# Performance work log

Hardware: AMD Instinct MI355X
Metric: run time of the kernel (lower is better)

Reference implementation:

```python
import jax, jax.numpy as jnp
import numpy as np
from jax import lax

IMG_SIZE = 640
STRIDES = (8, 16, 32)
NA = 3          # anchors per level
NC = 80         # classes
CONF_THRESH = 0.001
NMS_THRESH = 0.6
ANCHORS = np.array([[10,13],[16,30],[33,23],[30,61],[62,45],[59,119],[116,90],[156,198],[373,326]], np.float32).reshape(3, 3, 2)

def _make_grids():
    gs, st, aw = [], [], []
    for i, s in enumerate(STRIDES):
        hs = ws = IMG_SIZE // s
        gy, gx = np.meshgrid(np.arange(hs), np.arange(ws), indexing='ij')
        gxy = np.stack([gx, gy], -1).astype(np.float32).reshape(1, hs*ws, 1, 2)
        gs.append(gxy)
        st.append(np.full((1, hs*ws, NA, 2), s, np.float32))
        aw.append(np.tile(ANCHORS[i][None], (hs*ws, 1, 1)))
    return (np.concatenate(gs, 1), np.concatenate(st, 1), np.concatenate(aw, 0)[None])

GRID_CELL, STRIDE_T, ANCH_WH = _make_grids()  # [1,HW,1,2], [1,HW,3,2], [1,HW,3,2]

def _nms_classaware(boxes, score, valid):
    # Greedy NMS, class-aware via coordinate offset already applied to boxes.
    # Faithful to the numpy baseline: w,h = max(1e-28, .), areas without +1.
    x1, y1, x2, y2 = boxes[:, 0], boxes[:, 1], boxes[:, 2], boxes[:, 3]
    areas = (x2 - x1) * (y2 - y1)
    order = jnp.argsort(-score)
    N = boxes.shape[0]
    def body(i, state):
        supp, keep = state
        idx = order[i]
        active = jnp.logical_and(jnp.logical_not(supp[idx]), valid[idx])
        keep = keep.at[idx].set(active)
        xx1 = jnp.maximum(x1[idx], x1)
        yy1 = jnp.maximum(y1[idx], y1)
        xx2 = jnp.minimum(x2[idx], x2)
        yy2 = jnp.minimum(y2[idx], y2)
        w = jnp.maximum(1e-28, xx2 - xx1)
        h = jnp.maximum(1e-28, yy2 - yy1)
        inter = w * h
        iou = inter / (areas[idx] + areas - inter)
        newsupp = jnp.logical_and(iou > NMS_THRESH, active)
        newsupp = newsupp.at[idx].set(False)
        return jnp.logical_or(supp, newsupp), keep
    supp0 = jnp.zeros((N,), bool)
    keep0 = jnp.zeros((N,), bool)
    _, keep = lax.fori_loop(0, N, body, (supp0, keep0))
    return keep

def _decode_and_nms(pred_s, pred_m, pred_l):
    objs, clss, regs = [], [], []
    for pred in (pred_s, pred_m, pred_l):
        B, C, H, W = pred.shape
        p = pred.transpose(0, 2, 3, 1).reshape(B, H*W, C)
        objs.append(p[..., :NA].reshape(B, H*W*NA, 1))
        clss.append(p[..., NA:NA*(1+NC)].reshape(B, H*W*NA, NC))
        regs.append(p[..., NA*(1+NC):].reshape(B, H*W, NA, 4))
    obj_pred = jnp.concatenate(objs, axis=1)   # [B, N, 1]
    cls_pred = jnp.concatenate(clss, axis=1)   # [B, N, NC]
    reg_pred = jnp.concatenate(regs, axis=1)   # [B, HW, 3, 4]
    grid = jnp.asarray(GRID_CELL)
    stride = jnp.asarray(STRIDE_T)
    anch = jnp.asarray(ANCH_WH)
    B = reg_pred.shape[0]
    c_xy = (jax.nn.sigmoid(reg_pred[..., :2]) + grid) * stride
    b_wh = jnp.exp(reg_pred[..., 2:]) * anch
    xywh = jnp.concatenate([c_xy, b_wh], -1).reshape(B, -1, 4)
    x1y1 = xywh[..., :2] - xywh[..., 2:] / 2
    x2y2 = xywh[..., :2] + xywh[..., 2:] / 2
    boxes = jnp.clip(jnp.concatenate([x1y1, x2y2], -1) / IMG_SIZE, 0.0, 1.0)[0]  # [N,4]
    obj_s = jax.nn.sigmoid(obj_pred)[0]                     # [N,1]
    scores_all = jax.nn.softmax(cls_pred[0], axis=1) * obj_s  # [N,NC]
    cls_ind = jnp.argmax(scores_all, axis=1)                # [N]
    score = jnp.max(scores_all, axis=1)                     # [N]
    valid = score >= CONF_THRESH
    # class-aware NMS: offset normalized boxes by 2*class so classes never overlap
    boxes_off = boxes + cls_ind[:, None].astype(boxes.dtype) * 2.0
    keep = _nms_classaware(lax.stop_gradient(boxes_off), lax.stop_gradient(score), valid)
    out = jnp.concatenate([
        boxes,                                    # 4 cols
        score[:, None],                           # 1 col
        cls_ind[:, None].astype(boxes.dtype),     # 1 col (non-diff)
        keep[:, None].astype(boxes.dtype),        # 1 col (non-diff)
    ], axis=1)                                    # [N, 7]
    return out

def setup_inputs() -> dict:
    key = jax.random.key(0)
    k1, k2, k3 = jax.random.split(key, 3)
    return {
        'pred_s': jax.random.normal(k1, (1, 255, 80, 80), jnp.float32),
        'pred_m': jax.random.normal(k2, (1, 255, 40, 40), jnp.float32),
        'pred_l': jax.random.normal(k3, (1, 255, 20, 20), jnp.float32),
    }

def reference(pred_s, pred_m, pred_l):
    return _decode_and_nms(pred_s, pred_m, pred_l)
```

## Files before the change

kernel.cpp:

```cpp
#include <hip/hip_runtime.h>
#include <cstdint>

#define NPRED 25200
#define NPOS  8400
#define NCLS  80
#define CAP   512
#define MW    8
#define NCHUNK 132

__device__ __forceinline__ float sigmoidf_(float x) { return 1.0f / (1.0f + expf(-x)); }

__global__ __launch_bounds__(64) void decode_kernel(
    const float* __restrict__ ps, const float* __restrict__ pm, const float* __restrict__ pl,
    float* __restrict__ out,
    float4* __restrict__ g_boxin, uint64_t* __restrict__ g_key)
{
    int chunk = blockIdx.x;
    int a     = blockIdx.y;
    int t     = threadIdx.x;

    const float* p; int HW, W, base, si; float stride; int w0;
    if (chunk < 100)      { p = ps; HW = 6400; W = 80; stride = 8.f;  base = 0;    si = 0; w0 = chunk * 64; }
    else if (chunk < 125) { p = pm; HW = 1600; W = 40; stride = 16.f; base = 6400; si = 1; w0 = (chunk - 100) * 64; }
    else                  { p = pl; HW = 400;  W = 20; stride = 32.f; base = 8000; si = 2; w0 = (chunk - 125) * 64; }

    int local = w0 + t;
    bool valid = local < HW;
    int lclamp = valid ? local : (HW - 1);

    __shared__ float lds[NCLS * 64];

    const float* cbase = p + (size_t)(3 + a * NCLS) * HW;
    int lane_c = t >> 4;
    int j      = (t & 15) << 2;
    int off    = w0 + j; if (off > HW - 4) off = HW - 4;

    float4 vreg[20];
#pragma unroll
    for (int r0 = 0; r0 < 20; r0++)
        vreg[r0] = *(const float4*)(cbase + (size_t)(r0 * 4 + lane_c) * HW + off);
    float objl = p[(size_t)a * HW + lclamp];
    const float* rb = p + (size_t)(3 + 3 * NCLS + a * 4) * HW + lclamp;
    float tx = rb[0], ty = rb[(size_t)HW], tw = rb[(size_t)2 * HW], th = rb[(size_t)3 * HW];
#pragma unroll
    for (int r0 = 0; r0 < 20; r0++)
        *(float4*)&lds[(r0 * 4 + lane_c) * 64 + j] = vreg[r0];
    __syncthreads();

    float m = -INFINITY;
#pragma unroll 16
    for (int c = 0; c < NCLS; c++) m = fmaxf(m, lds[c * 64 + t]);
    float s = 0.f; float beste = -1.f; int bi = 0;
#pragma unroll 16
    for (int c = 0; c < NCLS; c++) {
        float e = expf(lds[c * 64 + t] - m);
        s += e;
        if (e > beste) { beste = e; bi = c; }
    }
    float obj = sigmoidf_(objl);
    float best = beste / s * obj;

    if (!valid) return;

    const float AW[9] = {10.f,16.f,33.f, 30.f,62.f,59.f, 116.f,156.f,373.f};
    const float AH[9] = {13.f,30.f,23.f, 61.f,45.f,119.f, 90.f,198.f,326.f};
    float aw = AW[si*3 + a], ah = AH[si*3 + a];

    int y = local / W;
    int x = local - y * W;
    float cx = (sigmoidf_(tx) + (float)x) * stride;
    float cy = (sigmoidf_(ty) + (float)y) * stride;
    float bw = expf(tw) * aw;
    float bh = expf(th) * ah;
    float x1 = fminf(fmaxf((cx - bw / 2.f) / 640.f, 0.f), 1.f);
    float y1 = fminf(fmaxf((cy - bh / 2.f) / 640.f, 0.f), 1.f);
    float x2 = fminf(fmaxf((cx + bw / 2.f) / 640.f, 0.f), 1.f);
    float y2 = fminf(fmaxf((cy + bh / 2.f) / 640.f, 0.f), 1.f);

    int g = (base + local) * 3 + a;
    float clsf = (float)bi;
    float* o = out + (size_t)g * 7;
    o[0] = x1; o[1] = y1; o[2] = x2; o[3] = y2;
    o[4] = best; o[5] = clsf; o[6] = 0.f;

    if (best >= 0.001f) {
        float off2 = clsf * 2.0f;
        g_boxin[g] = make_float4(x1 + off2, y1 + off2, x2 + off2, y2 + off2);
        unsigned u = __float_as_uint(best);
        u = (u & 0x80000000u) ? ~u : (u | 0x80000000u);
        g_key[g] = ((uint64_t)bi << 47) | ((uint64_t)(~u) << 15) | (uint64_t)g;
    } else {
        g_key[g] = (uint64_t)127 << 47;
    }
}

__global__ __launch_bounds__(1024, 4) void nms_fused_kernel(
    const uint64_t* __restrict__ g_key, const float4* __restrict__ g_boxin,
    float* __restrict__ out)
{
    int c = blockIdx.x;
    int tid = threadIdx.x;

    __shared__ uint64_t key_s[CAP];
    __shared__ float4   boxu_s[CAP];
    __shared__ float4   sbox_s[CAP + 64];
    __shared__ int      sg_s[CAP];
    __shared__ uint64_t mask_s[MW * CAP];
    __shared__ int      ln_s;

    if (tid == 0) ln_s = 0;
    __syncthreads();

    {
        int lane = tid & 63;
        const ulonglong2* kp = (const ulonglong2*)g_key;
        for (int idx = tid; idx < NPRED / 2; idx += 1024) {
            ulonglong2 kv = kp[idx];
            bool m0 = (int)(kv.x >> 47) == c;
            bool m1 = (int)(kv.y >> 47) == c;
            unsigned long long b0 = __ballot(m0);
            unsigned long long b1 = __ballot(m1);
            int total = __popcll(b0) + __popcll(b1);
            int base = 0;
            if (lane == 0 && total) base = atomicAdd(&ln_s, total);
            base = __shfl(base, 0);
            unsigned long long lower = ((unsigned long long)1 << lane) - 1;
            int off0 = base + __popcll(b0 & lower);
            int off1 = base + __popcll(b0) + __popcll(b1 & lower);
            if (m0 && off0 < CAP) key_s[off0] = kv.x;
            if (m1 && off1 < CAP) key_s[off1] = kv.y;
        }
    }
    __syncthreads();
    int n = ln_s; if (n > CAP) n = CAP;
    if (n == 0) return;
    int nw = (n + 63) >> 6;

    for (int i = tid; i < n; i += 1024)
        boxu_s[i] = g_boxin[key_s[i] & 0x7FFF];
    for (int i = n + tid; i < n + 64; i += 1024)
        sbox_s[i] = make_float4(3e30f, 3e30f, 3e30f, 3e30f);
    __syncthreads();

    for (int i0 = 0; i0 < n; i0 += 256) {
        int item = i0 + (tid >> 2);
        int sub  = tid & 3;
        bool act = item < n;
        int r = 0;
        uint64_t k = 0;
        if (act) {
            k = key_s[item];
            int nq = (n + 3) >> 2;
            int lo = sub * nq; if (lo > n) lo = n;
            int hi = lo + nq;  if (hi > n) hi = n;
            int jj = lo;
            for (; jj + 8 <= hi; jj += 8) {
                int t0 = key_s[jj]   < k, t1 = key_s[jj+1] < k;
                int t2 = key_s[jj+2] < k, t3 = key_s[jj+3] < k;
                int t4 = key_s[jj+4] < k, t5 = key_s[jj+5] < k;
                int t6 = key_s[jj+6] < k, t7 = key_s[jj+7] < k;
                r += t0 + t1 + t2 + t3 + t4 + t5 + t6 + t7;
            }
            for (; jj < hi; jj++) r += (key_s[jj] < k);
        }
        r += __shfl_xor(r, 1);
        r += __shfl_xor(r, 2);
        if (act && sub == 0) {
            sbox_s[r] = boxu_s[item];
            sg_s[r]   = (int)(k & 0x7FFF);
        }
    }
    __syncthreads();

    {
        int wid   = tid >> 6;
        int lane2 = tid & 63;
        int T = nw * (nw + 1) / 2;
        for (int t = wid; t < T; t += 16) {
            int w = 0, acc = 0;
            while (t >= acc + w + 1) { acc += w + 1; w++; }
            int ib = t - acc;
            int i  = (ib << 6) + lane2;
            float4 b4 = sbox_s[i];
            float Ai = (b4.z - b4.x) * (b4.w - b4.y);
            int j0 = w << 6;
            uint64_t bits = 0;
#pragma unroll 8
            for (int jq = 0; jq < 64; jq++) {
                float4 bj = sbox_s[j0 + jq];
                float xx1 = fmaxf(b4.x, bj.x);
                float yy1 = fmaxf(b4.y, bj.y);
                float xx2 = fminf(b4.z, bj.z);
                float yy2 = fminf(b4.w, bj.w);
                float ww = fmaxf(1e-28f, xx2 - xx1);
                float hh = fmaxf(1e-28f, yy2 - yy1);
                float inter = ww * hh;
                float Aj = (bj.z - bj.x) * (bj.w - bj.y);
                float iou = inter / ((Ai + Aj) - inter);
                if ((j0 + jq) > i && iou > 0.6f) bits |= 1ull << jq;
            }
            if (i < n) mask_s[w * CAP + i] = bits;
        }
    }
    __syncthreads();

    if (tid >= 64) return;
    int lane = tid;
    uint64_t removed = 0;
    for (int w = 0; w < nw; w++) {
        uint64_t rw = __shfl(removed, w);
        int row = (w << 6) + lane;
        uint64_t diag = (row < n) ? mask_s[w * CAP + row] : 0ull;
        int rem = n - (w << 6);
        uint64_t valid = (rem >= 64) ? ~0ull : ((1ull << rem) - 1ull);
        uint64_t nulls = __ballot(diag == 0ull);
        uint64_t cand = ~rw & valid;
        uint64_t kw = 0;
        uint64_t it = cand & ~nulls;
        while (it) {
            int b = __ffsll((unsigned long long)it) - 1;
            kw |= 1ull << b;
            uint64_t db = __shfl(diag, b);
            it &= ~db; cand &= ~db;
            it &= ~(1ull << b);
        }
        kw |= cand & nulls;

        int g  = lane >> 3;
        int wp = lane & 7;
        uint64_t acc = 0;
        if (wp >= w && wp < nw) {
            uint64_t mybits = kw & (0xFFull << (g * 8));
            while (mybits) {
                int b = __ffsll((unsigned long long)mybits) - 1;
                mybits &= mybits - 1;
                acc |= mask_s[wp * CAP + ((w << 6) + b)];
            }
        }
        acc |= __shfl_xor(acc, 8);
        acc |= __shfl_xor(acc, 16);
        acc |= __shfl_xor(acc, 32);
        if (lane < MW) removed |= acc;

        if (row < n && ((kw >> lane) & 1))
            out[(size_t)sg_s[row] * 7 + 6] = 1.0f;
    }
}

extern "C" void kernel_launch(void* const* d_in, const int* in_sizes, int n_in,
                              void* d_out, int out_size, void* d_ws, size_t ws_size,
                              hipStream_t stream) {
    const float* ps = (const float*)d_in[0];
    const float* pm = (const float*)d_in[1];
    const float* pl = (const float*)d_in[2];
    float* out = (float*)d_out;

    char* ws = (char*)d_ws;
    float4*   g_boxin = (float4*)ws;
    uint64_t* g_key   = (uint64_t*)(ws + 409600);

    decode_kernel<<<dim3(NCHUNK, 3), 64, 0, stream>>>(ps, pm, pl, out, g_boxin, g_key);
    nms_fused_kernel<<<NCLS, 1024, 0, stream>>>(g_key, g_boxin, out);
}
```

Measured before the change: 108.3 us.

## Load class logits directly to registers and micro-optimize NMS bucketing, ranking, masks

```diff
diff --git a/kernel.cpp b/kernel.cpp
--- a/kernel.cpp
+++ b/kernel.cpp
@@ -10,7 +10,7 @@
 
 __device__ __forceinline__ float sigmoidf_(float x) { return 1.0f / (1.0f + expf(-x)); }
 
-__global__ __launch_bounds__(64) void decode_kernel(
+__global__ __launch_bounds__(64, 2) void decode_kernel(
     const float* __restrict__ ps, const float* __restrict__ pm, const float* __restrict__ pl,
     float* __restrict__ out,
     float4* __restrict__ g_boxin, uint64_t* __restrict__ g_key)
@@ -28,32 +28,22 @@
     bool valid = local < HW;
     int lclamp = valid ? local : (HW - 1);
 
-    __shared__ float lds[NCLS * 64];
-
-    const float* cbase = p + (size_t)(3 + a * NCLS) * HW;
-    int lane_c = t >> 4;
-    int j      = (t & 15) << 2;
-    int off    = w0 + j; if (off > HW - 4) off = HW - 4;
-
-    float4 vreg[20];
-#pragma unroll
-    for (int r0 = 0; r0 < 20; r0++)
-        vreg[r0] = *(const float4*)(cbase + (size_t)(r0 * 4 + lane_c) * HW + off);
+    const float* cbase = p + (size_t)(3 + a * NCLS) * HW + lclamp;
+    float v[NCLS];
+#pragma unroll
+    for (int c = 0; c < NCLS; c++) v[c] = cbase[(size_t)c * HW];
+
     float objl = p[(size_t)a * HW + lclamp];
     const float* rb = p + (size_t)(3 + 3 * NCLS + a * 4) * HW + lclamp;
     float tx = rb[0], ty = rb[(size_t)HW], tw = rb[(size_t)2 * HW], th = rb[(size_t)3 * HW];
-#pragma unroll
-    for (int r0 = 0; r0 < 20; r0++)
-        *(float4*)&lds[(r0 * 4 + lane_c) * 64 + j] = vreg[r0];
-    __syncthreads();
 
     float m = -INFINITY;
-#pragma unroll 16
-    for (int c = 0; c < NCLS; c++) m = fmaxf(m, lds[c * 64 + t]);
+#pragma unroll
+    for (int c = 0; c < NCLS; c++) m = fmaxf(m, v[c]);
     float s = 0.f; float beste = -1.f; int bi = 0;
-#pragma unroll 16
+#pragma unroll
     for (int c = 0; c < NCLS; c++) {
-        float e = expf(lds[c * 64 + t] - m);
+        float e = expf(v[c] - m);
         s += e;
         if (e > beste) { beste = e; bi = c; }
     }
@@ -94,6 +84,23 @@
     }
 }
 
+#define BUCKET2(kv)                                                       \
+    {                                                                     \
+        bool m0 = (int)((kv).x >> 47) == c;                               \
+        bool m1 = (int)((kv).y >> 47) == c;                               \
+        unsigned long long b0 = __ballot(m0);                             \
+        unsigned long long b1 = __ballot(m1);                             \
+        int total = __popcll(b0) + __popcll(b1);                          \
+        int bs = 0;                                                       \
+        if (lane == 0 && total) bs = atomicAdd(&ln_s, total);             \
+        bs = __shfl(bs, 0);                                               \
+        unsigned long long lower = ((unsigned long long)1 << lane) - 1;   \
+        int off0 = bs + __popcll(b0 & lower);                             \
+        int off1 = bs + __popcll(b0) + __popcll(b1 & lower);              \
+        if (m0 && off0 < CAP) key_s[off0] = (kv).x;                       \
+        if (m1 && off1 < CAP) key_s[off1] = (kv).y;                       \
+    }
+
 __global__ __launch_bounds__(1024, 4) void nms_fused_kernel(
     const uint64_t* __restrict__ g_key, const float4* __restrict__ g_boxin,
     float* __restrict__ out)
@@ -101,7 +108,7 @@
     int c = blockIdx.x;
     int tid = threadIdx.x;
 
-    __shared__ uint64_t key_s[CAP];
+    __shared__ alignas(16) uint64_t key_s[CAP];
     __shared__ float4   boxu_s[CAP];
     __shared__ float4   sbox_s[CAP + 64];
     __shared__ int      sg_s[CAP];
@@ -114,21 +121,19 @@
     {
         int lane = tid & 63;
         const ulonglong2* kp = (const ulonglong2*)g_key;
-        for (int idx = tid; idx < NPRED / 2; idx += 1024) {
-            ulonglong2 kv = kp[idx];
-            bool m0 = (int)(kv.x >> 47) == c;
-            bool m1 = (int)(kv.y >> 47) == c;
-            unsigned long long b0 = __ballot(m0);
-            unsigned long long b1 = __ballot(m1);
-            int total = __popcll(b0) + __popcll(b1);
-            int base = 0;
-            if (lane == 0 && total) base = atomicAdd(&ln_s, total);
-            base = __shfl(base, 0);
-            unsigned long long lower = ((unsigned long long)1 << lane) - 1;
-            int off0 = base + __popcll(b0 & lower);
-            int off1 = base + __popcll(b0) + __popcll(b1 & lower);
-            if (m0 && off0 < CAP) key_s[off0] = kv.x;
-            if (m1 && off1 < CAP) key_s[off1] = kv.y;
+        const int HALF = NPRED / 2;
+        const int R2 = HALF >> 11;
+        for (int r = 0; r < R2; r++) {
+            int i0 = (r << 11) + tid;
+            ulonglong2 ka = kp[i0];
+            ulonglong2 kb = kp[i0 + 1024];
+            BUCKET2(ka);
+            BUCKET2(kb);
+        }
+        int ti = (R2 << 11) + tid;
+        if (ti < HALF) {
+            ulonglong2 ka = kp[ti];
+            BUCKET2(ka);
         }
     }
     __syncthreads();
@@ -150,18 +155,23 @@
         uint64_t k = 0;
         if (act) {
             k = key_s[item];
-            int nq = (n + 3) >> 2;
+            int nq = (((n + 3) >> 2) + 1) & ~1;
             int lo = sub * nq; if (lo > n) lo = n;
             int hi = lo + nq;  if (hi > n) hi = n;
             int jj = lo;
             for (; jj + 8 <= hi; jj += 8) {
-                int t0 = key_s[jj]   < k, t1 = key_s[jj+1] < k;
-                int t2 = key_s[jj+2] < k, t3 = key_s[jj+3] < k;
-                int t4 = key_s[jj+4] < k, t5 = key_s[jj+5] < k;
-                int t6 = key_s[jj+6] < k, t7 = key_s[jj+7] < k;
-                r += t0 + t1 + t2 + t3 + t4 + t5 + t6 + t7;
-            }
-            for (; jj < hi; jj++) r += (key_s[jj] < k);
+                ulonglong2 p0 = *(const ulonglong2*)&key_s[jj];
+                ulonglong2 p1 = *(const ulonglong2*)&key_s[jj + 2];
+                ulonglong2 p2 = *(const ulonglong2*)&key_s[jj + 4];
+                ulonglong2 p3 = *(const ulonglong2*)&key_s[jj + 6];
+                r += (p0.x < k) + (p0.y < k) + (p1.x < k) + (p1.y < k)
+                   + (p2.x < k) + (p2.y < k) + (p3.x < k) + (p3.y < k);
+            }
+            for (; jj + 2 <= hi; jj += 2) {
+                ulonglong2 p0 = *(const ulonglong2*)&key_s[jj];
+                r += (p0.x < k) + (p0.y < k);
+            }
+            if (jj < hi) r += (key_s[jj] < k);
         }
         r += __shfl_xor(r, 1);
         r += __shfl_xor(r, 2);
@@ -184,20 +194,22 @@
             float4 b4 = sbox_s[i];
             float Ai = (b4.z - b4.x) * (b4.w - b4.y);
             int j0 = w << 6;
+            float4 bjc = sbox_s[j0];
             uint64_t bits = 0;
 #pragma unroll 8
             for (int jq = 0; jq < 64; jq++) {
-                float4 bj = sbox_s[j0 + jq];
-                float xx1 = fmaxf(b4.x, bj.x);
-                float yy1 = fmaxf(b4.y, bj.y);
-                float xx2 = fminf(b4.z, bj.z);
-                float yy2 = fminf(b4.w, bj.w);
+                float4 bjn = sbox_s[j0 + ((jq + 1) & 63)];
+                float xx1 = fmaxf(b4.x, bjc.x);
+                float yy1 = fmaxf(b4.y, bjc.y);
+                float xx2 = fminf(b4.z, bjc.z);
+                float yy2 = fminf(b4.w, bjc.w);
                 float ww = fmaxf(1e-28f, xx2 - xx1);
                 float hh = fmaxf(1e-28f, yy2 - yy1);
                 float inter = ww * hh;
-                float Aj = (bj.z - bj.x) * (bj.w - bj.y);
+                float Aj = (bjc.z - bjc.x) * (bjc.w - bjc.y);
                 float iou = inter / ((Ai + Aj) - inter);
                 if ((j0 + jq) > i && iou > 0.6f) bits |= 1ull << jq;
+                bjc = bjn;
             }
             if (i < n) mask_s[w * CAP + i] = bits;
         }
@@ -230,11 +242,11 @@
         int wp = lane & 7;
         uint64_t acc = 0;
         if (wp >= w && wp < nw) {
-            uint64_t mybits = kw & (0xFFull << (g * 8));
-            while (mybits) {
-                int b = __ffsll((unsigned long long)mybits) - 1;
-                mybits &= mybits - 1;
-                acc |= mask_s[wp * CAP + ((w << 6) + b)];
+            int rbase = (w << 6) + (g << 3);
+#pragma unroll
+            for (int bb = 0; bb < 8; bb++) {
+                uint64_t mword = mask_s[wp * CAP + rbase + bb];
+                if ((kw >> ((g << 3) + bb)) & 1) acc |= mword;
             }
         }
         acc |= __shfl_xor(acc, 8);
```

Result: faster. 101.6 us (-6.2%).
